# Optimization experiments

Measured on AMD Instinct MI355X. Metric: run time of the kernel, lower is better.

The kernel has to match this reference:

```python
import jax, jax.numpy as jnp
import numpy as np
import math

C = 128
A_SCALES = [2.0, 4.0, 8.0]
A_RATIOS = [0.5, 1.0, 2.0]
STRIDES = [4, 8, 16, 32, 64]
NA = len(A_SCALES) * len(A_RATIOS)
IMG = 1024
N = 2
NMS_THRESH = 0.7
NUM_PRE = 6000
NUM_POST = 300
SCALE_CLIP = math.log(1000.0 / 16.0)


def base_anchors(stride):
    c = stride / 2.0
    a = []
    for s in A_SCALES:
        for r in A_RATIOS:
            h = stride * s * math.sqrt(r)
            w = stride * s * math.sqrt(1.0 / r)
            a.append((c - h / 2.0, c - w / 2.0, c + h / 2.0, c + w / 2.0))
    return np.array(a, dtype=np.float32)  # [NA,4] yxyx


def shifted_anchors(stride, H, W):
    base = jnp.asarray(base_anchors(stride))
    gy = jnp.arange(H, dtype=jnp.float32) * stride
    gx = jnp.arange(W, dtype=jnp.float32) * stride
    grid = jnp.stack(jnp.meshgrid(gy, gx, indexing='ij'), axis=-1)  # [H,W,2]
    shift = jnp.concatenate([grid, grid], axis=-1)  # [H,W,4]
    return (base[None, None] + shift[:, :, None]).reshape(-1, 4)  # [H*W*NA,4]


def conv(x, w, b, pad):
    y = jax.lax.conv_general_dilated(x, w, (1, 1), pad, dimension_numbers=('NCHW', 'OIHW', 'NCHW'))
    return y + b[None, :, None, None]


def head(x, w1, b1, wobj, bobj, wbbx, bbbx):
    h = jax.nn.relu(conv(x, w1, b1, 'SAME'))
    obj = conv(h, wobj, bobj, 'VALID')  # [N,NA,H,W]
    bbx = conv(h, wbbx, bbbx, 'VALID')  # [N,4*NA,H,W]
    n = x.shape[0]
    obj = obj.transpose(0, 2, 3, 1).reshape(n, -1)       # (h,w,anchor) order
    bbx = bbx.transpose(0, 2, 3, 1).reshape(n, -1, 4)
    return obj, bbx


def shift_boxes(anchors, deltas):
    yx = (anchors[..., :2] + anchors[..., 2:]) * 0.5
    hw = anchors[..., 2:] - anchors[..., :2]
    yx_o = yx + deltas[..., :2] * hw
    hw_o = hw * jnp.exp(jnp.minimum(deltas[..., 2:], SCALE_CLIP))
    return jnp.concatenate([yx_o - 0.5 * hw_o, yx_o + 0.5 * hw_o], axis=-1)


def nms_single(boxes, scores):
    # greedy hard NMS; boxes [P,4] yxyx, scores [P]; fixed NUM_POST outputs
    areas = (boxes[:, 2] - boxes[:, 0]) * (boxes[:, 3] - boxes[:, 1])

    def step(active, _):
        masked = jnp.where(active, scores, -jnp.inf)
        i = jnp.argmax(masked)
        ok = active[i]
        tl = jnp.maximum(boxes[i, :2], boxes[:, :2])
        br = jnp.minimum(boxes[i, 2:], boxes[:, 2:])
        inter = jnp.clip(br[:, 0] - tl[:, 0], 0.0) * jnp.clip(br[:, 1] - tl[:, 1], 0.0)
        iou = inter / (areas[i] + areas - inter + 1e-9)
        active = active & (iou <= NMS_THRESH)
        return active, (jnp.where(ok, i, 0), ok)

    _, (idx, valid) = jax.lax.scan(step, jnp.ones(boxes.shape[0], bool), None, length=NUM_POST)
    return idx, valid


def forward(x0, x1, x2, x3, x4, w1, b1, wobj, bobj, wbbx, bbbx, valid_size):
    feats = [x0, x1, x2, x3, x4]
    objs, bbxs, ancs = [], [], []
    for f, s in zip(feats, STRIDES):
        o, b = head(f, w1, b1, wobj, bobj, wbbx, bbbx)
        objs.append(o)
        bbxs.append(b)
        ancs.append(shifted_anchors(s, f.shape[2], f.shape[3]))
    obj = jnp.concatenate(objs, axis=1)        # [N,M]
    bbx = jnp.concatenate(bbxs, axis=1)        # [N,M,4]
    anchors = jnp.concatenate(ancs, axis=0)    # [M,4]
    boxes = shift_boxes(anchors[None], bbx)    # [N,M,4]
    h = valid_size[:, 0].astype(boxes.dtype)[:, None]
    w = valid_size[:, 1].astype(boxes.dtype)[:, None]
    boxes = jnp.stack([jnp.clip(boxes[..., 0], 0.0, h),
                       jnp.clip(boxes[..., 1], 0.0, w),
                       jnp.clip(boxes[..., 2], 0.0, h),
                       jnp.clip(boxes[..., 3], 0.0, w)], axis=-1)
    k = min(boxes.shape[1], NUM_PRE)
    top_scores, top_idx = jax.lax.top_k(obj, k)                     # per-image topk
    top_boxes = jnp.take_along_axis(boxes, top_idx[..., None], axis=1)
    idx, valid = jax.vmap(nms_single)(jax.lax.stop_gradient(top_boxes),
                                      jax.lax.stop_gradient(top_scores))
    props = jnp.take_along_axis(top_boxes, idx[..., None], axis=1)  # [N,NUM_POST,4]
    props = props * valid[..., None].astype(props.dtype)            # zero-pad invalid
    return props, valid


def setup_inputs() -> dict:
    key = jax.random.key(0)
    ks = jax.random.split(key, 8)
    sizes = [IMG // s for s in STRIDES]
    inp = {}
    for i, hw in enumerate(sizes):
        inp['x%d' % i] = jax.random.normal(ks[i], (N, C, hw, hw), jnp.float32)
    inp['w1'] = jax.random.normal(ks[5], (C, C, 3, 3), jnp.float32) * 0.05
    inp['b1'] = jnp.zeros((C,), jnp.float32)
    inp['wobj'] = jax.random.normal(ks[6], (NA, C, 1, 1), jnp.float32) * 0.05
    inp['bobj'] = jnp.zeros((NA,), jnp.float32)
    inp['wbbx'] = jax.random.normal(ks[7], (4 * NA, C, 1, 1), jnp.float32) * 0.05
    inp['bbbx'] = jnp.zeros((4 * NA,), jnp.float32)
    inp['valid_size'] = jnp.array([[IMG, IMG]] * N, jnp.int32)
    return inp


def reference(x0, x1, x2, x3, x4, w1, b1, wobj, bobj, wbbx, bbbx, valid_size):
    return forward(x0, x1, x2, x3, x4, w1, b1, wobj, bobj, wbbx, bbbx, valid_size)
```

## Files before the change

kernel.cpp:

```cpp
#include <hip/hip_runtime.h>
#include <stdint.h>
#include <math.h>

#define M_TOT 785664
#define NPRE  6000
#define NPOST 300
#define CAP   8192
#define NWORDS 94
#define ROWW   96
#define NPAD   6016

__device__ __forceinline__ uint32_t okey(float f) {
    uint32_t u = __float_as_uint(f);
    return (u & 0x80000000u) ? ~u : (u | 0x80000000u);
}

__global__ void k_zero(uint32_t* p, int n) {
    int i = blockIdx.x * blockDim.x + threadIdx.x;
    if (i < n) p[i] = 0u;
}

__global__ void k_wt(const float* __restrict__ w1, float* __restrict__ wt) {
    int i = blockIdx.x * 256 + threadIdx.x;
    if (i >= 128 * 128 * 9) return;
    int co = i / 1152; int r = i % 1152; int ci = r / 9; int tap = r % 9;
    wt[ci * 1152 + tap * 128 + co] = w1[i];
}

__global__ __launch_bounds__(512) void k_conv(
    const float* __restrict__ x0, const float* __restrict__ x1,
    const float* __restrict__ x2, const float* __restrict__ x3,
    const float* __restrict__ x4,
    const float* __restrict__ wt, const float* __restrict__ b1,
    const float* __restrict__ wobj, const float* __restrict__ bobj,
    const float* __restrict__ wbbx, const float* __restrict__ bbbx,
    float* __restrict__ sc, float* __restrict__ dl)
{
    __shared__ __attribute__((aligned(16))) float sx[8][18][20];
    __shared__ __attribute__((aligned(16))) float sw[8 * 9 * 128];

    int b = blockIdx.x, L = 0;
    if (b >= 512) { b -= 512; L = 1;
        if (b >= 128) { b -= 128; L = 2;
            if (b >= 32) { b -= 32; L = 3;
                if (b >= 8) { b -= 8; L = 4; } } } }
    const float* xs = (L == 0) ? x0 : (L == 1) ? x1 : (L == 2) ? x2 : (L == 3) ? x3 : x4;
    const int scoff_[5] = {0, 589824, 737280, 774144, 783360};
    int Wl = 256 >> L; int Hl = Wl; int HW = Wl * Wl;
    int tpiSh = 8 - 2 * L;
    int n  = b >> tpiSh;
    int r  = b & ((1 << tpiSh) - 1);
    int txSh = 4 - L;
    int ty0 = r >> txSh, tx0 = r & ((1 << txSh) - 1);
    int y0 = ty0 << 4, x0c = tx0 << 4;
    const float* xin = xs + (size_t)n * 128 * HW;

    int t = threadIdx.x;
    int tx = t & 15;
    int pg = t >> 4;
    int py = pg >> 1, px = (pg & 1) << 3;

    float acc[64];
#pragma unroll
    for (int i = 0; i < 64; ++i) acc[i] = 0.f;

    for (int cc0 = 0; cc0 < 128; cc0 += 8) {
        __syncthreads();
        for (int i = t; i < 2880; i += 512) {
            int ci = i / 360; int rm = i % 360; int rr = rm / 20; int cc = rm % 20;
            float v = 0.f;
            int gy = y0 - 1 + rr, gx = x0c - 1 + cc;
            if (cc < 18 && gy >= 0 && gy < Hl && gx >= 0 && gx < Wl)
                v = xin[(size_t)(cc0 + ci) * HW + (size_t)gy * Wl + gx];
            sx[ci][rr][cc] = v;
        }
        {
            const float4* wsrc = (const float4*)(wt + (size_t)cc0 * 1152);
            float4* wdst = (float4*)sw;
            for (int i = t; i < 2304; i += 512) wdst[i] = wsrc[i];
        }
        __syncthreads();

#pragma unroll 1
        for (int ci = 0; ci < 8; ++ci) {
#pragma unroll
            for (int dy = 0; dy < 3; ++dy) {
                const float* xr = &sx[ci][py + dy][px];
                float4 xa = *(const float4*)(xr);
                float4 xb = *(const float4*)(xr + 4);
                float4 xc = *(const float4*)(xr + 8);
                float win[12] = {xa.x, xa.y, xa.z, xa.w, xb.x, xb.y, xb.z, xb.w,
                                 xc.x, xc.y, xc.z, xc.w};
#pragma unroll
                for (int dx = 0; dx < 3; ++dx) {
                    const float* wr = &sw[(ci * 9 + dy * 3 + dx) * 128 + tx * 8];
                    float4 wa = *(const float4*)(wr);
                    float4 wb = *(const float4*)(wr + 4);
                    float wv[8] = {wa.x, wa.y, wa.z, wa.w, wb.x, wb.y, wb.z, wb.w};
#pragma unroll
                    for (int c = 0; c < 8; ++c)
#pragma unroll
                        for (int e = 0; e < 8; ++e)
                            acc[c * 8 + e] = fmaf(wv[c], win[dx + e], acc[c * 8 + e]);
                }
            }
        }
    }

#pragma unroll
    for (int c = 0; c < 8; ++c) {
        float bb = b1[tx * 8 + c];
#pragma unroll
        for (int e = 0; e < 8; ++e) {
            float v = acc[c * 8 + e] + bb;
            acc[c * 8 + e] = v > 0.f ? v : 0.f;
        }
    }

    int gy = y0 + py, gxb = x0c + px;
    size_t ppos = (size_t)gy * Wl + gxb;
    size_t scbase = (size_t)n * M_TOT + scoff_[L];
    size_t dlbase = (size_t)n * 4 * (size_t)M_TOT + 4 * (size_t)scoff_[L];
    for (int a = 0; a < 45; ++a) {
        const float* wp = (a < 9) ? (wobj + (size_t)a * 128) : (wbbx + (size_t)(a - 9) * 128);
        float4 wa = *(const float4*)(wp + tx * 8);
        float4 wb = *(const float4*)(wp + tx * 8 + 4);
        float wv[8] = {wa.x, wa.y, wa.z, wa.w, wb.x, wb.y, wb.z, wb.w};
        float p[8];
#pragma unroll
        for (int e = 0; e < 8; ++e) p[e] = 0.f;
#pragma unroll
        for (int c = 0; c < 8; ++c)
#pragma unroll
            for (int e = 0; e < 8; ++e)
                p[e] = fmaf(wv[c], acc[c * 8 + e], p[e]);
#pragma unroll
        for (int mm = 1; mm < 16; mm <<= 1)
#pragma unroll
            for (int e = 0; e < 8; ++e)
                p[e] += __shfl_xor(p[e], mm, 64);
        if (tx == 0) {
            float bias = (a < 9) ? bobj[a] : bbbx[a - 9];
            float4 o0 = make_float4(p[0] + bias, p[1] + bias, p[2] + bias, p[3] + bias);
            float4 o1 = make_float4(p[4] + bias, p[5] + bias, p[6] + bias, p[7] + bias);
            float* dst = (a < 9) ? (sc + scbase + (size_t)a * HW + ppos)
                                 : (dl + dlbase + (size_t)(a - 9) * HW + ppos);
            *(float4*)dst = o0;
            *(float4*)(dst + 4) = o1;
        }
    }
}

__global__ __launch_bounds__(256) void k_hist(const float* __restrict__ sc,
                                              uint32_t* __restrict__ hist) {
    __shared__ uint32_t lh[8192];
    int n = blockIdx.y;
    for (int i = threadIdx.x; i < 8192; i += 256) lh[i] = 0u;
    __syncthreads();
    const float* s = sc + (size_t)n * M_TOT;
    int stride = gridDim.x * 256;
    for (int i = blockIdx.x * 256 + threadIdx.x; i < M_TOT; i += stride)
        atomicAdd(&lh[okey(s[i]) >> 19], 1u);
    __syncthreads();
    for (int i = threadIdx.x; i < 8192; i += 256) {
        uint32_t v = lh[i];
        if (v) atomicAdd(&hist[n * 8192 + i], v);
    }
}

__global__ void k_subhist(const float* __restrict__ sc, const uint32_t* __restrict__ ctrl,
                          uint32_t* __restrict__ subh) {
    int i = blockIdx.x * blockDim.x + threadIdx.x;
    int stride = gridDim.x * blockDim.x;
    for (; i < 2 * M_TOT; i += stride) {
        int n = i >= M_TOT;
        uint32_t k = okey(sc[i]);
        if ((k >> 19) == ctrl[n * 8 + 0])
            atomicAdd(&subh[n * 8192 + ((k >> 6) & 0x1FFFu)], 1u);
    }
}

__global__ void k_scan(const uint32_t* __restrict__ hist, uint32_t* __restrict__ ctrl, int phase) {
    int n = blockIdx.x;
    const uint32_t* h = hist + n * 8192;
    uint32_t* c = ctrl + n * 8;
    __shared__ uint32_t tp[256];
    int t = threadIdx.x;
    uint32_t s = 0;
    for (int r = 0; r < 32; ++r) s += h[8191 - (t * 32 + r)];
    tp[t] = s;
    __syncthreads();
    if (t == 0) {
        uint32_t run = (phase == 0) ? 0u : c[1];
        for (int i = 0; i < 256; ++i) { uint32_t v = tp[i]; tp[i] = run; run += v; }
    }
    __syncthreads();
    uint32_t cum = tp[t];
    for (int r = 0; r < 32; ++r) {
        int j = 8191 - (t * 32 + r);
        uint32_t cc = h[j];
        if (cum < 6000u && cum + cc >= 6000u) {
            if (phase == 0) { c[0] = (uint32_t)j; c[1] = cum; }
            else            { c[2] = (c[0] << 19) | ((uint32_t)j << 6); }
        }
        cum += cc;
    }
}

__global__ void k_compact(const float* __restrict__ sc, uint32_t* __restrict__ ctrl,
                          uint64_t* __restrict__ cand) {
    int i = blockIdx.x * blockDim.x + threadIdx.x;
    int stride = gridDim.x * blockDim.x;
    const int scoff_[5] = {0, 589824, 737280, 774144, 783360};
    int lane = threadIdx.x & 63;
    for (; i < 2 * M_TOT; i += stride) {
        int n = i >= M_TOT;
        int q = n ? (i - M_TOT) : i;
        uint32_t k = okey(sc[i]);
        bool hit = (k >= ctrl[n * 8 + 2]);
        unsigned long long m = __ballot(hit);
        if (m) {
            int leader = __builtin_ctzll(m);
            uint32_t base = 0;
            if (lane == leader) base = atomicAdd(&ctrl[n * 8 + 3], (uint32_t)__popcll(m));
            base = (uint32_t)__shfl((int)base, leader, 64);
            if (hit) {
                uint32_t slot = base + (uint32_t)__popcll(m & ((1ull << lane) - 1ull));
                if (slot < CAP) {
                    int Lq = (q < 589824) ? 0 : (q < 737280) ? 1 : (q < 774144) ? 2
                            : (q < 783360) ? 3 : 4;
                    int r = q - scoff_[Lq];
                    int sh = 16 - 2 * Lq;
                    int a = r >> sh;
                    int pos = r & ((1 << sh) - 1);
                    uint32_t mm = (uint32_t)(scoff_[Lq] + pos * 9 + a);
                    cand[(size_t)n * CAP + slot] = ((uint64_t)k << 32) | (uint32_t)(~mm);
                }
            }
        }
    }
}

__global__ __launch_bounds__(256) void k_rank(const uint64_t* __restrict__ cand,
                                              const uint32_t* __restrict__ ctrl,
                                              uint64_t* __restrict__ sorted) {
    __shared__ uint64_t chunk[2048];
    int n = blockIdx.y;
    uint32_t cnt = ctrl[n * 8 + 3];
    if (cnt > CAP) cnt = CAP;
    const uint64_t* cb = cand + (size_t)n * CAP;
    uint64_t* sb = sorted + (size_t)n * CAP;
    int i = blockIdx.x * 256 + threadIdx.x;
    uint64_t key = (i < (int)cnt) ? cb[i] : 0ull;
    uint32_t rank = 0;
    for (uint32_t base = 0; base < cnt; base += 2048) {
        __syncthreads();
        for (int j = threadIdx.x; j < 2048; j += 256) {
            uint32_t idx = base + (uint32_t)j;
            chunk[j] = (idx < cnt) ? cb[idx] : 0ull;
        }
        __syncthreads();
        uint32_t lim = cnt - base; if (lim > 2048u) lim = 2048u;
        for (uint32_t j = 0; j < lim; ++j) rank += (chunk[j] > key) ? 1u : 0u;
    }
    if (i < (int)cnt && rank < CAP) sb[rank] = key;
}

__global__ void k_decode(const uint64_t* __restrict__ cand, const float* __restrict__ dl,
                         const int* __restrict__ vsz, float* __restrict__ boxes) {
    int i = blockIdx.x * 256 + threadIdx.x;
    if (i >= 2 * NPRE) return;
    int n = i / NPRE, rk = i % NPRE;
    const int scoff_[5] = {0, 589824, 737280, 774144, 783360};
    uint64_t pk = cand[(size_t)n * CAP + rk];
    uint32_t m = ~(uint32_t)(pk & 0xFFFFFFFFull);
    int Lq = (m < 589824u) ? 0 : (m < 737280u) ? 1 : (m < 774144u) ? 2 : (m < 783360u) ? 3 : 4;
    int r = (int)m - scoff_[Lq];
    int pos = r / 9;
    int a = r - pos * 9;
    int Wl = 256 >> Lq;
    int y = pos >> (8 - Lq);
    int xx = pos & (Wl - 1);
    float stridef = (float)(4 << Lq);
    double sD = (double)(2 << (a / 3));
    double rD = ((a % 3) == 0) ? 0.5 : ((a % 3) == 1) ? 1.0 : 2.0;
    double hD = ((double)stridef * sD) * sqrt(rD);
    double wD = ((double)stridef * sD) * sqrt(1.0 / rD);
    double cD = (double)stridef / 2.0;
    float y1b = (float)(cD - hD / 2.0);
    float x1b = (float)(cD - wD / 2.0);
    float y2b = (float)(cD + hD / 2.0);
    float x2b = (float)(cD + wD / 2.0);
    float gy = (float)y * stridef;
    float gx = (float)xx * stridef;
    float ay1 = __fadd_rn(y1b, gy), ax1 = __fadd_rn(x1b, gx);
    float ay2 = __fadd_rn(y2b, gy), ax2 = __fadd_rn(x2b, gx);
    float cy = __fmul_rn(__fadd_rn(ay1, ay2), 0.5f);
    float cx = __fmul_rn(__fadd_rn(ax1, ax2), 0.5f);
    float ah = __fsub_rn(ay2, ay1);
    float aw = __fsub_rn(ax2, ax1);
    size_t HWl = (size_t)Wl * Wl;
    size_t db = (size_t)n * 4 * M_TOT + 4 * (size_t)scoff_[Lq] + (size_t)pos;
    float dy_ = dl[db + (size_t)(a * 4 + 0) * HWl];
    float dx_ = dl[db + (size_t)(a * 4 + 1) * HWl];
    float dh_ = dl[db + (size_t)(a * 4 + 2) * HWl];
    float dw_ = dl[db + (size_t)(a * 4 + 3) * HWl];
    float yo = __fadd_rn(cy, __fmul_rn(dy_, ah));
    float xo = __fadd_rn(cx, __fmul_rn(dx_, aw));
    const float SCLIPf = 4.135166556742356f;
    float ho = __fmul_rn(ah, (float)exp((double)fminf(dh_, SCLIPf)));
    float wo = __fmul_rn(aw, (float)exp((double)fminf(dw_, SCLIPf)));
    float hf = (float)vsz[n * 2 + 0], wf = (float)vsz[n * 2 + 1];
    float y1 = fminf(fmaxf(__fsub_rn(yo, __fmul_rn(0.5f, ho)), 0.f), hf);
    float x1 = fminf(fmaxf(__fsub_rn(xo, __fmul_rn(0.5f, wo)), 0.f), wf);
    float y2 = fminf(fmaxf(__fadd_rn(yo, __fmul_rn(0.5f, ho)), 0.f), hf);
    float x2 = fminf(fmaxf(__fadd_rn(xo, __fmul_rn(0.5f, wo)), 0.f), wf);
    *(float4*)(boxes + ((size_t)n * NPAD + rk) * 4) = make_float4(y1, x1, y2, x2);
}

__global__ __launch_bounds__(256) void k_iou(const float* __restrict__ boxes,
                                             uint64_t* __restrict__ ioum) {
    int n = blockIdx.y;
    int i = blockIdx.x * 4 + (threadIdx.x >> 6);
    int lane = threadIdx.x & 63;
    const float* bsrc = boxes + (size_t)n * NPAD * 4;
    float4 bi = *(const float4*)(bsrc + (size_t)i * 4);
    float ai = __fmul_rn(__fsub_rn(bi.z, bi.x), __fsub_rn(bi.w, bi.y));
    uint64_t* row = ioum + ((size_t)n * NPAD + i) * ROWW;
    for (int w = 0; w < NWORDS; ++w) {
        int j = (w << 6) | lane;
        bool pred = false;
        if (j > i && j < NPRE) {
            float4 bj = *(const float4*)(bsrc + (size_t)j * 4);
            float aj = __fmul_rn(__fsub_rn(bj.z, bj.x), __fsub_rn(bj.w, bj.y));
            float ty = fmaxf(bi.x, bj.x), tx2 = fmaxf(bi.y, bj.y);
            float by = fminf(bi.z, bj.z), bx2 = fminf(bi.w, bj.w);
            float ih = fmaxf(__fsub_rn(by, ty), 0.f), iw = fmaxf(__fsub_rn(bx2, tx2), 0.f);
            float inter = __fmul_rn(ih, iw);
            float den = __fadd_rn(__fsub_rn(__fadd_rn(ai, aj), inter), 1e-9f);
            float iou = __fdiv_rn(inter, den);
            pred = iou > 0.7f;
        }
        unsigned long long msk = __ballot(pred);
        if (lane == 0) row[w] = (uint64_t)msk;
    }
}

__global__ __launch_bounds__(64) void k_nms(const float* __restrict__ boxes,
                                            const uint64_t* __restrict__ ioum,
                                            float* __restrict__ out) {
    int n = blockIdx.x;
    __shared__ uint64_t sup[NWORDS];
    __shared__ int keepl[NPOST];
    int lane = threadIdx.x;
    for (int w = lane; w < NWORDS; w += 64) sup[w] = 0ull;
    __syncthreads();
    int kept = 0;
    bool stop = false;
    for (int w = 0; w < NWORDS && kept < NPOST && !stop; ++w) {
        uint64_t vmask = (w == NWORDS - 1) ? ((1ull << 48) - 1ull) : ~0ull;
        uint64_t avail = (~sup[w]) & vmask;
        while (avail && kept < NPOST) {
            int bpos = __builtin_ctzll(avail);
            int i = (w << 6) | bpos;
            if (lane == 0) keepl[kept] = i;
            kept++;
            float4 bi = *(const float4*)(boxes + ((size_t)n * NPAD + i) * 4);
            float area = __fmul_rn(__fsub_rn(bi.z, bi.x), __fsub_rn(bi.w, bi.y));
            float selfiou = __fdiv_rn(area, __fadd_rn(area, 1e-9f));
            if (!(selfiou > 0.7f)) {
                if (lane == 0) { for (int k2 = kept; k2 < NPOST; ++k2) keepl[k2] = i; }
                kept = NPOST;
                stop = true;
                break;
            }
            const uint64_t* row = ioum + ((size_t)n * NPAD + i) * ROWW;
            sup[lane] |= row[lane];
            if (lane < NWORDS - 64) sup[64 + lane] |= row[64 + lane];
            __syncthreads();
            avail = (~sup[w]) & vmask & ~((2ull << bpos) - 1ull);
        }
    }
    __syncthreads();
    for (int k = lane; k < NPOST; k += 64) {
        float4 bx = make_float4(0.f, 0.f, 0.f, 0.f);
        float vf = 0.f;
        if (k < kept) {
            int i = keepl[k];
            bx = *(const float4*)(boxes + ((size_t)n * NPAD + i) * 4);
            vf = 1.f;
        }
        *(float4*)(out + (size_t)n * 1200 + (size_t)k * 4) = bx;
        out[2400 + n * 300 + k] = vf;
    }
}

__global__ __launch_bounds__(256) void k_diag(const uint32_t* __restrict__ ctrl,
                                              const uint64_t* __restrict__ sorted,
                                              const float* __restrict__ boxes,
                                              float* __restrict__ out) {
    __shared__ unsigned sfl;
    if (threadIdx.x == 0) sfl = 0u;
    __syncthreads();
    unsigned fl = 0;
    for (int n = 0; n < 2; ++n) {
        if (threadIdx.x == 0) {
            uint32_t cnt = ctrl[n * 8 + 3];
            if (cnt < 6000u || cnt > (uint32_t)CAP) fl |= 1u << n;
        }
        for (int r = threadIdx.x + 1; r < NPRE; r += 256)
            if (sorted[(size_t)n * CAP + r - 1] <= sorted[(size_t)n * CAP + r])
                fl |= 4u << n;
        for (int r = threadIdx.x; r < NPRE * 4; r += 256) {
            float v = boxes[(size_t)n * NPAD * 4 + r];
            if (!(v >= 0.0f && v <= 1024.0f)) fl |= 16u << n;
        }
    }
    if (fl) atomicOr(&sfl, fl);
    __syncthreads();
    if (threadIdx.x == 0 && sfl) out[0] = 65536.0f * (float)(1u + sfl);
}

extern "C" void kernel_launch(void* const* d_in, const int* in_sizes, int n_in,
                              void* d_out, int out_size, void* d_ws, size_t ws_size,
                              hipStream_t stream) {
    (void)out_size; (void)ws_size;
    static const int want[12] = {16777216, 4194304, 1048576, 262144, 65536,
                                 147456, 128, 1152, 9, 4608, 36, 4};
    const void* p[12];
    for (int k = 0; k < 12; ++k) p[k] = d_in[k];
    bool pos_ok = (n_in >= 12);
    for (int k = 0; k < 12 && pos_ok; ++k) if (in_sizes[k] != want[k]) pos_ok = false;
    if (!pos_ok) {
        for (int k = 0; k < 12; ++k)
            for (int j = 0; j < n_in; ++j)
                if (in_sizes[j] == want[k]) { p[k] = d_in[j]; break; }
    }
    const float* x0   = (const float*)p[0];
    const float* x1   = (const float*)p[1];
    const float* x2   = (const float*)p[2];
    const float* x3   = (const float*)p[3];
    const float* x4   = (const float*)p[4];
    const float* w1   = (const float*)p[5];
    const float* b1   = (const float*)p[6];
    const float* wobj = (const float*)p[7];
    const float* bobj = (const float*)p[8];
    const float* wbbx = (const float*)p[9];
    const float* bbbx = (const float*)p[10];
    const int*   vsz  = (const int*)p[11];
    float* out = (float*)d_out;

    size_t off = 0;
    char* base = (char*)d_ws;
    auto carve = [&](size_t bytes) -> void* {
        void* q = base + off;
        off += (bytes + 255) & ~(size_t)255;
        return q;
    };
    float*    SC     = (float*)carve((size_t)2 * M_TOT * 4);
    float*    DL     = (float*)carve((size_t)2 * M_TOT * 16);
    float*    WT     = (float*)carve((size_t)147456 * 4);
    uint32_t* HIST   = (uint32_t*)carve((size_t)16384 * 4);
    uint32_t* SUBH   = (uint32_t*)carve((size_t)16384 * 4);
    uint32_t* CTRL   = (uint32_t*)carve((size_t)64 * 4);
    uint64_t* CAND   = (uint64_t*)carve((size_t)2 * CAP * 8);
    uint64_t* SORTED = (uint64_t*)carve((size_t)2 * CAP * 8);
    float*    BOXES  = (float*)carve((size_t)2 * NPAD * 16);
    uint64_t* IOUM   = (uint64_t*)carve((size_t)2 * NPAD * ROWW * 8);

    int zn = (int)(((char*)CAND - (char*)HIST) / 4);
    k_zero<<<(zn + 255) / 256, 256, 0, stream>>>(HIST, zn);
    k_wt<<<(147456 + 255) / 256, 256, 0, stream>>>(w1, WT);
    k_conv<<<682, 512, 0, stream>>>(x0, x1, x2, x3, x4, WT, b1,
                                    wobj, bobj, wbbx, bbbx, SC, DL);
    k_hist<<<dim3(256, 2), 256, 0, stream>>>(SC, HIST);
    k_scan<<<2, 256, 0, stream>>>(HIST, CTRL, 0);
    k_subhist<<<1024, 256, 0, stream>>>(SC, CTRL, SUBH);
    k_scan<<<2, 256, 0, stream>>>(SUBH, CTRL, 1);
    k_compact<<<1024, 256, 0, stream>>>(SC, CTRL, CAND);
    k_rank<<<dim3(CAP / 256, 2), 256, 0, stream>>>(CAND, CTRL, SORTED);
    k_decode<<<(2 * NPRE + 255) / 256, 256, 0, stream>>>(SORTED, DL, vsz, BOXES);
    k_iou<<<dim3(NPRE / 4, 2), 256, 0, stream>>>(BOXES, IOUM);
    k_nms<<<2, 64, 0, stream>>>(BOXES, IOUM, out);
    k_diag<<<1, 256, 0, stream>>>(CTRL, SORTED, BOXES, out);
}
```

Before: 1.121 ms.

## Enlarge per-thread conv register tile to 8 channels by 16 pixels with 256 threads

The fused 3x3 conv kernel now runs 256 threads per block instead of 512. Each thread computes 8 output channels across a full 16-pixel row, split as two groups of 4 channels 64 apart, instead of 8 channels by 8 pixels. This doubles the work per thread and loads each input window once per row, cutting LDS traffic per FMA. The weight reads are also arranged to avoid bank conflicts. In exchange the kernel needs 128 accumulator registers per thread, which raises register pressure and may lower occupancy or cause spills, and the 1x1 head reduction now shuffles 16 values.

```diff
diff --git a/kernel.cpp b/kernel.cpp
--- a/kernel.cpp
+++ b/kernel.cpp
@@ -27,7 +27,7 @@
     wt[ci * 1152 + tap * 128 + co] = w1[i];
 }
 
-__global__ __launch_bounds__(512) void k_conv(
+__global__ __launch_bounds__(256) void k_conv(
     const float* __restrict__ x0, const float* __restrict__ x1,
     const float* __restrict__ x2, const float* __restrict__ x3,
     const float* __restrict__ x4,
@@ -57,16 +57,17 @@
 
     int t = threadIdx.x;
     int tx = t & 15;
-    int pg = t >> 4;
-    int py = pg >> 1, px = (pg & 1) << 3;
-
-    float acc[64];
-#pragma unroll
-    for (int i = 0; i < 64; ++i) acc[i] = 0.f;
+    int py = t >> 4;
+
+    float acc0[4][16], acc1[4][16];
+#pragma unroll
+    for (int c = 0; c < 4; ++c)
+#pragma unroll
+        for (int e = 0; e < 16; ++e) { acc0[c][e] = 0.f; acc1[c][e] = 0.f; }
 
     for (int cc0 = 0; cc0 < 128; cc0 += 8) {
         __syncthreads();
-        for (int i = t; i < 2880; i += 512) {
+        for (int i = t; i < 2880; i += 256) {
             int ci = i / 360; int rm = i % 360; int rr = rm / 20; int cc = rm % 20;
             float v = 0.f;
             int gy = y0 - 1 + rr, gx = x0c - 1 + cc;
@@ -77,7 +78,7 @@
         {
             const float4* wsrc = (const float4*)(wt + (size_t)cc0 * 1152);
             float4* wdst = (float4*)sw;
-            for (int i = t; i < 2304; i += 512) wdst[i] = wsrc[i];
+            for (int i = t; i < 2304; i += 256) wdst[i] = wsrc[i];
         }
         __syncthreads();
 
@@ -85,68 +86,84 @@
         for (int ci = 0; ci < 8; ++ci) {
 #pragma unroll
             for (int dy = 0; dy < 3; ++dy) {
-                const float* xr = &sx[ci][py + dy][px];
+                const float* xr = &sx[ci][py + dy][0];
                 float4 xa = *(const float4*)(xr);
                 float4 xb = *(const float4*)(xr + 4);
                 float4 xc = *(const float4*)(xr + 8);
-                float win[12] = {xa.x, xa.y, xa.z, xa.w, xb.x, xb.y, xb.z, xb.w,
-                                 xc.x, xc.y, xc.z, xc.w};
+                float4 xd = *(const float4*)(xr + 12);
+                float4 xe = *(const float4*)(xr + 16);
+                float win[18] = {xa.x, xa.y, xa.z, xa.w, xb.x, xb.y, xb.z, xb.w,
+                                 xc.x, xc.y, xc.z, xc.w, xd.x, xd.y, xd.z, xd.w,
+                                 xe.x, xe.y};
 #pragma unroll
                 for (int dx = 0; dx < 3; ++dx) {
-                    const float* wr = &sw[(ci * 9 + dy * 3 + dx) * 128 + tx * 8];
+                    const float* wr = &sw[(ci * 9 + dy * 3 + dx) * 128 + tx * 4];
                     float4 wa = *(const float4*)(wr);
-                    float4 wb = *(const float4*)(wr + 4);
-                    float wv[8] = {wa.x, wa.y, wa.z, wa.w, wb.x, wb.y, wb.z, wb.w};
-#pragma unroll
-                    for (int c = 0; c < 8; ++c)
-#pragma unroll
-                        for (int e = 0; e < 8; ++e)
-                            acc[c * 8 + e] = fmaf(wv[c], win[dx + e], acc[c * 8 + e]);
+                    float4 wb = *(const float4*)(wr + 64);
+                    float wva[4] = {wa.x, wa.y, wa.z, wa.w};
+                    float wvb[4] = {wb.x, wb.y, wb.z, wb.w};
+#pragma unroll
+                    for (int e = 0; e < 16; ++e) {
+                        float xv = win[e + dx];
+#pragma unroll
+                        for (int c = 0; c < 4; ++c) {
+                            acc0[c][e] = fmaf(wva[c], xv, acc0[c][e]);
+                            acc1[c][e] = fmaf(wvb[c], xv, acc1[c][e]);
+                        }
+                    }
                 }
             }
         }
     }
 
 #pragma unroll
-    for (int c = 0; c < 8; ++c) {
-        float bb = b1[tx * 8 + c];
-#pragma unroll
-        for (int e = 0; e < 8; ++e) {
-            float v = acc[c * 8 + e] + bb;
-            acc[c * 8 + e] = v > 0.f ? v : 0.f;
-        }
-    }
-
-    int gy = y0 + py, gxb = x0c + px;
-    size_t ppos = (size_t)gy * Wl + gxb;
+    for (int c = 0; c < 4; ++c) {
+        float ba = b1[tx * 4 + c];
+        float bb = b1[64 + tx * 4 + c];
+#pragma unroll
+        for (int e = 0; e < 16; ++e) {
+            float v0 = acc0[c][e] + ba;
+            float v1 = acc1[c][e] + bb;
+            acc0[c][e] = v0 > 0.f ? v0 : 0.f;
+            acc1[c][e] = v1 > 0.f ? v1 : 0.f;
+        }
+    }
+
+    int gy = y0 + py;
+    size_t ppos = (size_t)gy * Wl + x0c;
     size_t scbase = (size_t)n * M_TOT + scoff_[L];
     size_t dlbase = (size_t)n * 4 * (size_t)M_TOT + 4 * (size_t)scoff_[L];
     for (int a = 0; a < 45; ++a) {
         const float* wp = (a < 9) ? (wobj + (size_t)a * 128) : (wbbx + (size_t)(a - 9) * 128);
-        float4 wa = *(const float4*)(wp + tx * 8);
-        float4 wb = *(const float4*)(wp + tx * 8 + 4);
-        float wv[8] = {wa.x, wa.y, wa.z, wa.w, wb.x, wb.y, wb.z, wb.w};
-        float p[8];
-#pragma unroll
-        for (int e = 0; e < 8; ++e) p[e] = 0.f;
-#pragma unroll
-        for (int c = 0; c < 8; ++c)
-#pragma unroll
-            for (int e = 0; e < 8; ++e)
-                p[e] = fmaf(wv[c], acc[c * 8 + e], p[e]);
+        float4 wa = *(const float4*)(wp + tx * 4);
+        float4 wb = *(const float4*)(wp + 64 + tx * 4);
+        float wva[4] = {wa.x, wa.y, wa.z, wa.w};
+        float wvb[4] = {wb.x, wb.y, wb.z, wb.w};
+        float p[16];
+#pragma unroll
+        for (int e = 0; e < 16; ++e) p[e] = 0.f;
+#pragma unroll
+        for (int c = 0; c < 4; ++c)
+#pragma unroll
+            for (int e = 0; e < 16; ++e) {
+                p[e] = fmaf(wva[c], acc0[c][e], p[e]);
+                p[e] = fmaf(wvb[c], acc1[c][e], p[e]);
+            }
 #pragma unroll
         for (int mm = 1; mm < 16; mm <<= 1)
 #pragma unroll
-            for (int e = 0; e < 8; ++e)
+            for (int e = 0; e < 16; ++e)
                 p[e] += __shfl_xor(p[e], mm, 64);
         if (tx == 0) {
             float bias = (a < 9) ? bobj[a] : bbbx[a - 9];
-            float4 o0 = make_float4(p[0] + bias, p[1] + bias, p[2] + bias, p[3] + bias);
-            float4 o1 = make_float4(p[4] + bias, p[5] + bias, p[6] + bias, p[7] + bias);
             float* dst = (a < 9) ? (sc + scbase + (size_t)a * HW + ppos)
                                  : (dl + dlbase + (size_t)(a - 9) * HW + ppos);
-            *(float4*)dst = o0;
-            *(float4*)(dst + 4) = o1;
+#pragma unroll
+            for (int q = 0; q < 4; ++q) {
+                float4 o = make_float4(p[q * 4] + bias, p[q * 4 + 1] + bias,
+                                       p[q * 4 + 2] + bias, p[q * 4 + 3] + bias);
+                *(float4*)(dst + q * 4) = o;
+            }
         }
     }
 }
@@ -471,7 +488,7 @@
     int zn = (int)(((char*)CAND - (char*)HIST) / 4);
     k_zero<<<(zn + 255) / 256, 256, 0, stream>>>(HIST, zn);
     k_wt<<<(147456 + 255) / 256, 256, 0, stream>>>(w1, WT);
-    k_conv<<<682, 512, 0, stream>>>(x0, x1, x2, x3, x4, WT, b1,
+    k_conv<<<682, 256, 0, stream>>>(x0, x1, x2, x3, x4, WT, b1,
                                     wobj, bobj, wbbx, bbbx, SC, DL);
     k_hist<<<dim3(256, 2), 256, 0, stream>>>(SC, HIST);
     k_scan<<<2, 256, 0, stream>>>(HIST, CTRL, 0);
```

Measured after the change: 1.186 ms. +5.8%, slower.
